# Optimization experiments

Hardware: AMD Instinct MI355X
Metric: run time of the kernel (lower is better)

## Reference

```python
import jax, jax.numpy as jnp
import numpy as np

N_F = 256
D = 4 * N_F          # d_model after PixelUnshuffle(2)
D_INNER = 2 * D      # mamba expand=2
D_STATE = 16
DT_RANK = D // 16
N_LAYERS = 8
BATCH = 16
IMG = 32


def _pixel_unshuffle(x, r):
    b, c, h, w = x.shape
    x = x.reshape(b, c, h // r, r, w // r, r)
    return x.transpose(0, 1, 3, 5, 2, 4).reshape(b, c * r * r, h // r, w // r)


def _pixel_shuffle(x, r):
    b, c, h, w = x.shape
    co = c // (r * r)
    x = x.reshape(b, co, r, r, h, w)
    return x.transpose(0, 1, 4, 2, 5, 3).reshape(b, co, h * r, w * r)


def _layernorm(x, w, b):
    mu = jnp.mean(x, -1, keepdims=True)
    var = jnp.mean((x - mu) ** 2, -1, keepdims=True)
    return (x - mu) * jax.lax.rsqrt(var + 1e-5) * w + b


def _transpose_xy(a):
    b, l, c = a.shape
    s = int(np.sqrt(l))
    return a.reshape(b, s, s, c).transpose(0, 2, 1, 3).reshape(b, l, c)


def _mamba_mixer(u, W_in_i, conv_w_i, conv_b_i, W_x_i, W_dt_i, b_dt_i, A_log_i, D_skip_i, W_out_i):
    b, l, d = u.shape
    xz = jnp.einsum('bld,ed->ble', u, W_in_i)          # (B,L,2*d_inner)
    x, z = jnp.split(xz, 2, axis=-1)
    # causal depthwise conv over sequence, kernel 4, left-pad 3
    xt = jax.lax.conv_general_dilated(
        x.transpose(0, 2, 1), conv_w_i[:, None, :], (1,), [(3, 0)],
        feature_group_count=D_INNER, dimension_numbers=('NCH', 'OIH', 'NCH'))
    x = jax.nn.silu((xt + conv_b_i[None, :, None]).transpose(0, 2, 1))  # (B,L,d_inner)
    dbc = jnp.einsum('ble,fe->blf', x, W_x_i)          # (B,L,dt_rank+2*d_state)
    dt = jax.nn.softplus(jnp.einsum('blr,er->ble', dbc[..., :DT_RANK], W_dt_i) + b_dt_i)
    Bm = dbc[..., DT_RANK:DT_RANK + D_STATE]
    Cm = dbc[..., DT_RANK + D_STATE:]
    A = -jnp.exp(A_log_i)                              # (d_inner, d_state)

    def step(h, inp):
        dt_t, B_t, C_t, x_t = inp                      # (B,di),(B,ds),(B,ds),(B,di)
        h = jnp.exp(dt_t[..., None] * A) * h + (dt_t * x_t)[..., None] * B_t[:, None, :]
        return h, jnp.einsum('bds,bs->bd', h, C_t)

    h0 = jnp.zeros((b, D_INNER, D_STATE), dtype=u.dtype)
    _, ys = jax.lax.scan(step, h0, (dt.transpose(1, 0, 2), Bm.transpose(1, 0, 2),
                                    Cm.transpose(1, 0, 2), x.transpose(1, 0, 2)))
    y = ys.transpose(1, 0, 2) + x * D_skip_i
    y = y * jax.nn.silu(z)
    return jnp.einsum('ble,de->bld', y, W_out_i)


def setup_inputs() -> dict:
    key = jax.random.key(0)
    ks = jax.random.split(key, 20)
    s = 0.02
    inp = {
        'x': jax.random.normal(ks[0], (BATCH, 3, IMG, IMG), jnp.float32),
        'noise_level': jax.random.uniform(ks[1], (BATCH, 1, 1, 1), jnp.float32),
        'pe_w1': jax.random.normal(ks[2], (N_F, 4), jnp.float32) * s,
        'pe_b1': jnp.zeros((N_F,), jnp.float32),
        'pe_w2': jax.random.normal(ks[3], (N_F, N_F), jnp.float32) * s,
        'ln_w': jnp.ones((N_LAYERS, D), jnp.float32),
        'ln_b': jnp.zeros((N_LAYERS, D), jnp.float32),
        'W_in': jax.random.normal(ks[4], (N_LAYERS, 2 * D_INNER, D), jnp.float32) * s,
        'conv_w': jax.random.normal(ks[5], (N_LAYERS, D_INNER, 4), jnp.float32) * s,
        'conv_b': jnp.zeros((N_LAYERS, D_INNER), jnp.float32),
        'W_x': jax.random.normal(ks[6], (N_LAYERS, DT_RANK + 2 * D_STATE, D_INNER), jnp.float32) * s,
        'W_dt': jax.random.normal(ks[7], (N_LAYERS, D_INNER, DT_RANK), jnp.float32) * s,
        'b_dt': jax.random.normal(ks[8], (N_LAYERS, D_INNER), jnp.float32) * s,
        'A_log': jnp.broadcast_to(jnp.log(jnp.arange(1, D_STATE + 1, dtype=jnp.float32)),
                                  (N_LAYERS, D_INNER, D_STATE)),
        'D_skip': jnp.ones((N_LAYERS, D_INNER), jnp.float32),
        'W_out': jax.random.normal(ks[9], (N_LAYERS, D, D_INNER), jnp.float32) * s,
        'op_w1': jax.random.normal(ks[10], (4 * N_F, 12 * N_F), jnp.float32) * s,
        'op_b1': jnp.zeros((4 * N_F,), jnp.float32),
        'op_w2': jax.random.normal(ks[11], (3, N_F), jnp.float32) * s,
        'op_b2': jnp.zeros((3,), jnp.float32),
    }
    return inp


def reference(x, noise_level, pe_w1, pe_b1, pe_w2, ln_w, ln_b, W_in, conv_w, conv_b,
              W_x, W_dt, b_dt, A_log, D_skip, W_out, op_w1, op_b1, op_w2, op_b2):
    B, _, H, W = x.shape
    nl = jnp.broadcast_to(noise_level, (B, 1, H, W))
    h = jnp.concatenate([x, nl], axis=1)                       # (B,4,H,W)
    h = jax.nn.relu(jnp.einsum('bchw,oc->bohw', h, pe_w1) + pe_b1[None, :, None, None])
    h = jnp.einsum('bchw,oc->bohw', h, pe_w2)
    X = _pixel_unshuffle(h, 2)                                 # (B,4*n_f,H/2,W/2)
    Bc, C, Hh, Ww = X.shape
    y = X.reshape(Bc, C, Hh * Ww).transpose(0, 2, 1)           # (B,L,d_model)
    z = None
    for i in range(N_LAYERS):
        z = y if z is None else y + z                          # Block residual routing
        yn = _layernorm(z, ln_w[i], ln_b[i])
        y = _mamba_mixer(yn, W_in[i], conv_w[i], conv_b[i], W_x[i], W_dt[i], b_dt[i],
                         A_log[i], D_skip[i], W_out[i])
        y = _transpose_xy(y)
        z = _transpose_xy(z)
        if (i + 1) % 4 == 0:
            y = y[:, ::-1]
            z = z[:, ::-1]
    y2 = y.transpose(0, 2, 1).reshape(X.shape)
    z2 = z.transpose(0, 2, 1).reshape(X.shape)
    out = jnp.concatenate([X, y2, z2], axis=1)                 # (B,12*n_f,H/2,W/2)
    out = jax.nn.relu(jnp.einsum('bchw,oc->bohw', out, op_w1) + op_b1[None, :, None, None])
    out = _pixel_shuffle(out, 2)                               # (B,n_f,H,W)
    out = jnp.einsum('bchw,oc->bohw', out, op_w2) + op_b2[None, :, None, None]
    return out
```

## Files before the change

kernel.cpp:

```cpp
#include <hip/hip_runtime.h>

typedef unsigned short u16;
typedef __bf16 bf16x8 __attribute__((ext_vector_type(8)));
typedef float f32x4 __attribute__((ext_vector_type(4)));
typedef const __attribute__((address_space(1))) void* as1p;
typedef __attribute__((address_space(3))) void* as3p;

#define VMCNT4 asm volatile("s_waitcnt vmcnt(4)" ::: "memory")
#define LGKM0  asm volatile("s_waitcnt lgkmcnt(0)" ::: "memory")

__device__ __forceinline__ float bf2f(u16 h) { return __uint_as_float(((unsigned)h) << 16); }
__device__ __forceinline__ float ldf(const void* p, size_t i, int bf) {
    return bf ? bf2f(((const u16*)p)[i]) : ((const float*)p)[i];
}
__device__ __forceinline__ float4 ldf4(const void* p, size_t i, int bf) {
    if (bf) {
        const u16* q = (const u16*)p + i;
        ushort4 v = *(const ushort4*)q;
        return make_float4(bf2f(v.x), bf2f(v.y), bf2f(v.z), bf2f(v.w));
    }
    return *(const float4*)((const float*)p + i);
}
__device__ __forceinline__ u16 f2bf(float f) {
    unsigned u = __float_as_uint(f);
    unsigned r = (u + 0x7FFFu + ((u >> 16) & 1u)) >> 16;
    return (u16)r;
}
__device__ __forceinline__ float silu_f(float x) { return x * (1.f / (1.f + __expf(-x))); }

__device__ __forceinline__ int permL(int l, int rev) {
    if (rev) l = 255 - l;
    return ((l & 15) << 4) | (l >> 4);
}

__device__ __forceinline__ void gload_lds16(const void* g, void* l) {
    __builtin_amdgcn_global_load_lds((as1p)g, (as3p)l, 16, 0, 0);
}

__global__ void k_detect(const void* lnw, int* flag) {
    if (threadIdx.x == 0 && blockIdx.x == 0) {
        unsigned w = ((const unsigned*)lnw)[0];
        *flag = (w == 0x3F803F80u) ? 1 : 0;
    }
}

__global__ void k_cvt(const void* src, size_t soff, u16* __restrict__ dst, int n,
                      const int* __restrict__ flagp) {
    int bf = *flagp;
    int i4 = (blockIdx.x * 256 + threadIdx.x) * 4;
    if (i4 >= n) return;
    float4 v = ldf4(src, soff + i4, bf);
    *(ushort4*)(dst + i4) = make_ushort4(f2bf(v.x), f2bf(v.y), f2bf(v.z), f2bf(v.w));
}

__global__ void k_cvt_padx(const void* src, u16* __restrict__ dst,
                           const int* __restrict__ flagp) {
    int bf = *flagp;
    int i4 = (blockIdx.x * 256 + threadIdx.x) * 4;
    int row = i4 >> 11, col = i4 & 2047;
    int layer = row >> 7, lrow = row & 127;
    ushort4 o = make_ushort4(0, 0, 0, 0);
    if (lrow < 96) {
        float4 v = ldf4(src, (size_t)layer * 96 * 2048 + (size_t)lrow * 2048 + col, bf);
        o = make_ushort4(f2bf(v.x), f2bf(v.y), f2bf(v.z), f2bf(v.w));
    }
    *(ushort4*)(dst + i4) = o;
}

__global__ void k_head1(const void* x, const void* nl, const void* w1, const void* b1,
                        float* __restrict__ h1, const int* flagp) {
    int bf = *flagp;
    int idx = blockIdx.x * 256 + threadIdx.x;
    int o = idx & 255, p = (idx >> 8) & 1023, b = idx >> 18;
    float c0 = ldf(x, ((size_t)b * 3 + 0) * 1024 + p, bf);
    float c1 = ldf(x, ((size_t)b * 3 + 1) * 1024 + p, bf);
    float c2 = ldf(x, ((size_t)b * 3 + 2) * 1024 + p, bf);
    float c3 = ldf(nl, b, bf);
    float acc = ldf(w1, (size_t)o * 4 + 0, bf) * c0 + ldf(w1, (size_t)o * 4 + 1, bf) * c1 +
                ldf(w1, (size_t)o * 4 + 2, bf) * c2 + ldf(w1, (size_t)o * 4 + 3, bf) * c3 +
                ldf(b1, o, bf);
    h1[idx] = fmaxf(acc, 0.f);
}

template <int EPI>
__global__ __launch_bounds__(256) void k_gemm(
    const float* __restrict__ A, int lda,
    const void* __restrict__ W, size_t woff,
    const void* __restrict__ bias, size_t boff,
    float* __restrict__ C, int N, int K,
    const int* __restrict__ flagp, int perm) {
    int bf = *flagp;
    __shared__ float As[16][68];
    __shared__ float Ws[16][68];
    int t = threadIdx.x;
    int m0 = blockIdx.y * 64, n0 = blockIdx.x * 64;
    int lrow = t >> 2, lcol = (t & 3) << 2;
    int tx = t & 15, tyr = t >> 4;
    float acc[4][4] = {};
    for (int k0 = 0; k0 < K; k0 += 16) {
        float4 av = *(const float4*)(A + (size_t)(m0 + lrow) * lda + k0 + lcol);
        float4 wv = make_float4(0.f, 0.f, 0.f, 0.f);
        int nrow = n0 + lrow;
        if (nrow < N) wv = ldf4(W, woff + (size_t)nrow * K + k0 + lcol, bf);
        __syncthreads();
        As[lcol + 0][lrow] = av.x; As[lcol + 1][lrow] = av.y;
        As[lcol + 2][lrow] = av.z; As[lcol + 3][lrow] = av.w;
        Ws[lcol + 0][lrow] = wv.x; Ws[lcol + 1][lrow] = wv.y;
        Ws[lcol + 2][lrow] = wv.z; Ws[lcol + 3][lrow] = wv.w;
        __syncthreads();
#pragma unroll
        for (int k = 0; k < 16; ++k) {
            float4 a = *(const float4*)&As[k][tyr << 2];
            float4 bv = *(const float4*)&Ws[k][tx << 2];
            float aa[4] = {a.x, a.y, a.z, a.w};
            float bb[4] = {bv.x, bv.y, bv.z, bv.w};
#pragma unroll
            for (int i = 0; i < 4; ++i)
#pragma unroll
                for (int j = 0; j < 4; ++j) acc[i][j] += aa[i] * bb[j];
        }
    }
#pragma unroll
    for (int i = 0; i < 4; ++i) {
        int m = m0 + (tyr << 2) + i;
        int mo = m;
        if (perm >= 0) { int b = m >> 8, l = m & 255; mo = (b << 8) | permL(l, perm); }
#pragma unroll
        for (int j = 0; j < 4; ++j) {
            int n = n0 + (tx << 2) + j;
            if (n >= N) continue;
            float v = acc[i][j];
            if (EPI == 1) { v += ldf(bias, boff + n, bf); v = fmaxf(v, 0.f); }
            if (EPI == 2) { v += ldf(bias, boff + n, bf); v = (v > 20.f) ? v : log1pf(expf(v)); }
            C[(size_t)mo * N + n] = v;
        }
    }
}

template <int OUT16>
__global__ __launch_bounds__(512, 2) void k_m256(
    const u16* __restrict__ A, int lda,
    const u16* __restrict__ W, int ldw,
    void* __restrict__ Cv, int ldc, int ktPerZ) {
    __shared__ __align__(16) u16 Ab[2][2][128 * 64];
    __shared__ __align__(16) u16 Bb[2][2][128 * 64];
    int t = threadIdx.x;
    int w = t >> 6, lane = t & 63;
    int wm = w >> 2, wn = w & 3;
    int fr = lane & 15, q = lane >> 4;
    int flat = blockIdx.y * gridDim.x + blockIdx.x;
    int nwg = gridDim.x * gridDim.y, cpx = nwg >> 3;
    int tile = (flat & 7) * cpx + (flat >> 3);
    int bx = tile % gridDim.x, by = tile / gridDim.x;
    int m0 = by * 256, n0 = bx * 256;
    int kt0 = blockIdx.z * ktPerZ;
    int sr = t >> 3, sslot = t & 7;

    auto stA = [&](int d, int kt, int h, int j) {
        int lr = j * 64 + sr;
        int gr = (lr >> 6) * 128 + h * 64 + (lr & 63);
        int col = kt * 64 + ((sslot ^ (lr & 7)) << 3);
        gload_lds16(A + (size_t)(m0 + gr) * lda + col, &Ab[d][h][lr * 64 + sslot * 8]);
    };
    auto stB = [&](int d, int kt, int h, int j) {
        int lr = j * 64 + sr;
        int gr = (lr >> 5) * 64 + h * 32 + (lr & 31);
        int col = kt * 64 + ((sslot ^ (lr & 7)) << 3);
        gload_lds16(W + (size_t)(n0 + gr) * ldw + col, &Bb[d][h][lr * 64 + sslot * 8]);
    };
    auto ldA = [&](int d, int mf, int kk) {
        int lr = wm * 64 + (mf & 3) * 16 + fr;
        int sl = (kk * 4 + q) ^ (lr & 7);
        return *(const bf16x8*)&Ab[d][mf >> 2][lr * 64 + sl * 8];
    };
    auto ldB = [&](int d, int nf, int kk) {
        int lr = wn * 32 + (nf & 1) * 16 + fr;
        int sl = (kk * 4 + q) ^ (lr & 7);
        return *(const bf16x8*)&Bb[d][nf >> 1][lr * 64 + sl * 8];
    };

    f32x4 acc[8][4] = {};
    bf16x8 av[4][2], bv0[2][2], bv1[2][2];

    stA(0, kt0, 0, 0); stA(0, kt0, 0, 1); stA(0, kt0, 1, 0); stA(0, kt0, 1, 1);
    stB(0, kt0, 0, 0); stB(0, kt0, 0, 1); stB(0, kt0, 1, 0); stB(0, kt0, 1, 1);
    asm volatile("s_waitcnt vmcnt(0)" ::: "memory");
    __builtin_amdgcn_s_barrier();

    for (int kt = kt0; kt < kt0 + ktPerZ; ++kt) {
        int d = (kt - kt0) & 1, nd = d ^ 1, nk = kt + 1;
        bool more = nk < kt0 + ktPerZ;
        VMCNT4;
        __builtin_amdgcn_s_barrier();
        if (more) { stA(nd, nk, 0, 0); stA(nd, nk, 0, 1); }
#pragma unroll
        for (int m = 0; m < 4; ++m) { av[m][0] = ldA(d, m, 0); av[m][1] = ldA(d, m, 1); }
#pragma unroll
        for (int n = 0; n < 2; ++n) { bv0[n][0] = ldB(d, n, 0); bv0[n][1] = ldB(d, n, 1); }
        LGKM0; __builtin_amdgcn_sched_barrier(0);
        __builtin_amdgcn_s_setprio(1);
#pragma unroll
        for (int m = 0; m < 4; ++m)
#pragma unroll
            for (int n = 0; n < 2; ++n) {
                acc[m][n] = __builtin_amdgcn_mfma_f32_16x16x32_bf16(av[m][0], bv0[n][0], acc[m][n], 0, 0, 0);
                acc[m][n] = __builtin_amdgcn_mfma_f32_16x16x32_bf16(av[m][1], bv0[n][1], acc[m][n], 0, 0, 0);
            }
        __builtin_amdgcn_s_setprio(0);
        VMCNT4;
        __builtin_amdgcn_s_barrier();
        if (more) { stB(nd, nk, 0, 0); stB(nd, nk, 0, 1); }
#pragma unroll
        for (int n = 0; n < 2; ++n) { bv1[n][0] = ldB(d, n + 2, 0); bv1[n][1] = ldB(d, n + 2, 1); }
        LGKM0; __builtin_amdgcn_sched_barrier(0);
        __builtin_amdgcn_s_setprio(1);
#pragma unroll
        for (int m = 0; m < 4; ++m)
#pragma unroll
            for (int n = 0; n < 2; ++n) {
                acc[m][n + 2] = __builtin_amdgcn_mfma_f32_16x16x32_bf16(av[m][0], bv1[n][0], acc[m][n + 2], 0, 0, 0);
                acc[m][n + 2] = __builtin_amdgcn_mfma_f32_16x16x32_bf16(av[m][1], bv1[n][1], acc[m][n + 2], 0, 0, 0);
            }
        __builtin_amdgcn_s_setprio(0);
        VMCNT4;
        __builtin_amdgcn_s_barrier();
        if (more) { stB(nd, nk, 1, 0); stB(nd, nk, 1, 1); }
#pragma unroll
        for (int m = 0; m < 4; ++m) { av[m][0] = ldA(d, m + 4, 0); av[m][1] = ldA(d, m + 4, 1); }
        LGKM0; __builtin_amdgcn_sched_barrier(0);
        __builtin_amdgcn_s_setprio(1);
#pragma unroll
        for (int m = 0; m < 4; ++m)
#pragma unroll
            for (int n = 0; n < 2; ++n) {
                acc[m + 4][n] = __builtin_amdgcn_mfma_f32_16x16x32_bf16(av[m][0], bv0[n][0], acc[m + 4][n], 0, 0, 0);
                acc[m + 4][n] = __builtin_amdgcn_mfma_f32_16x16x32_bf16(av[m][1], bv0[n][1], acc[m + 4][n], 0, 0, 0);
            }
        __builtin_amdgcn_s_setprio(0);
        VMCNT4;
        __builtin_amdgcn_s_barrier();
        if (more) { stA(nd, nk, 1, 0); stA(nd, nk, 1, 1); }
        __builtin_amdgcn_s_setprio(1);
#pragma unroll
        for (int m = 0; m < 4; ++m)
#pragma unroll
            for (int n = 0; n < 2; ++n) {
                acc[m + 4][n + 2] = __builtin_amdgcn_mfma_f32_16x16x32_bf16(av[m][0], bv1[n][0], acc[m + 4][n + 2], 0, 0, 0);
                acc[m + 4][n + 2] = __builtin_amdgcn_mfma_f32_16x16x32_bf16(av[m][1], bv1[n][1], acc[m + 4][n + 2], 0, 0, 0);
            }
        __builtin_amdgcn_s_setprio(0);
    }
    if (OUT16) {
        u16* Ch = (u16*)Cv;
#pragma unroll
        for (int m = 0; m < 8; ++m) {
            int row = m0 + wm * 128 + m * 16 + q * 4;
#pragma unroll
            for (int rr = 0; rr < 4; ++rr)
#pragma unroll
                for (int n = 0; n < 4; ++n)
                    Ch[(size_t)(row + rr) * ldc + n0 + wn * 64 + n * 16 + fr] = f2bf(acc[m][n][rr]);
        }
    } else {
        float* Cf = (float*)Cv + (size_t)blockIdx.z * (size_t)gridDim.y * 256 * ldc;
#pragma unroll
        for (int m = 0; m < 8; ++m) {
            int row = m0 + wm * 128 + m * 16 + q * 4;
#pragma unroll
            for (int rr = 0; rr < 4; ++rr)
#pragma unroll
                for (int n = 0; n < 4; ++n)
                    Cf[(size_t)(row + rr) * ldc + n0 + wn * 64 + n * 16 + fr] = acc[m][n][rr];
        }
    }
}

template <int EPI, int OUT16, int BN>
__global__ __launch_bounds__(256) void k_mgemm(
    const u16* __restrict__ A, int lda,
    const u16* __restrict__ W, int ldw,
    const void* __restrict__ bias, size_t boff,
    void* __restrict__ Cv, int ldc, int N,
    int ktPerZ, int perm, const int* __restrict__ flagp) {
    constexpr int NF = BN / 32;
    int bf = *flagp;
    __shared__ __align__(16) u16 As[128 * 32];
    __shared__ __align__(16) u16 Bs[BN * 32];
    int t = threadIdx.x;
    int gx = gridDim.x;
    int flat = blockIdx.y * gx + blockIdx.x;
    int nwg = gx * gridDim.y;
    if ((nwg & 7) == 0) {
        int cpx = nwg >> 3;
        flat = (flat & 7) * cpx + (flat >> 3);
    }
    int bx = flat % gx, by = flat / gx;
    int m0 = by * 128, n0 = bx * BN;
    int kt0 = blockIdx.z * ktPerZ;
    float* Cf = (float*)Cv + (size_t)blockIdx.z * (size_t)gridDim.y * 128 * ldc;
    u16* Ch = (u16*)Cv;
    int w = t >> 6, lane = t & 63;
    int wm = w >> 1, wn = w & 1;
    int fr = lane & 15, kb = (lane >> 4) * 8;
    int srow = lane >> 2, scol = (lane & 3) * 8;
    f32x4 acc[4][NF] = {};
    for (int kt = kt0; kt < kt0 + ktPerZ; ++kt) {
        int kc = kt * 32;
#pragma unroll
        for (int i = 0; i < 2; ++i) {
            int r = i * 64 + w * 16 + srow;
            gload_lds16(A + (size_t)(m0 + r) * lda + kc + scol, As + i * 2048 + w * 512);
        }
#pragma unroll
        for (int i = 0; i < BN / 64; ++i) {
            int r = i * 64 + w * 16 + srow;
            gload_lds16(W + (size_t)(n0 + r) * ldw + kc + scol, Bs + i * 2048 + w * 512);
        }
        __syncthreads();
        bf16x8 af[4], bv[NF];
#pragma unroll
        for (int m = 0; m < 4; ++m)
            af[m] = *(const bf16x8*)(As + (wm * 64 + m * 16 + fr) * 32 + kb);
#pragma unroll
        for (int n = 0; n < NF; ++n)
            bv[n] = *(const bf16x8*)(Bs + (wn * NF * 16 + n * 16 + fr) * 32 + kb);
#pragma unroll
        for (int m = 0; m < 4; ++m)
#pragma unroll
            for (int n = 0; n < NF; ++n)
                acc[m][n] = __builtin_amdgcn_mfma_f32_16x16x32_bf16(af[m], bv[n], acc[m][n], 0, 0, 0);
        __syncthreads();
    }
    int r0 = (lane >> 4) * 4;
#pragma unroll
    for (int m = 0; m < 4; ++m) {
        int rowb = m0 + wm * 64 + m * 16 + r0;
#pragma unroll
        for (int rr = 0; rr < 4; ++rr) {
            int row = rowb + rr;
            int mo = row;
            if (perm >= 0) { int bb = row >> 8, l = row & 255; mo = (bb << 8) | permL(l, perm); }
#pragma unroll
            for (int n = 0; n < NF; ++n) {
                int col = n0 + wn * NF * 16 + n * 16 + fr;
                if (col >= N) continue;
                float v = acc[m][n][rr];
                if (EPI == 1) { v += ldf(bias, boff + col, bf); v = fmaxf(v, 0.f); }
                if (EPI == 2) { v += ldf(bias, boff + col, bf); v = (v > 20.f) ? v : log1pf(expf(v)); }
                if (OUT16) Ch[(size_t)mo * ldc + col] = f2bf(v);
                else       Cf[(size_t)mo * ldc + col] = v;
            }
        }
    }
}

template <int EPI>
__global__ void k_ored(const float* __restrict__ part, float* __restrict__ out,
                       const void* __restrict__ bias,
                       const int* __restrict__ flagp, int perm, int nz) {
    int bf = *flagp;
    int idx4 = (blockIdx.x * 256 + threadIdx.x) * 4;
    int m = idx4 >> 10, n = idx4 & 1023;
    float4 s = make_float4(0.f, 0.f, 0.f, 0.f);
    for (int z = 0; z < nz; ++z) {
        float4 p = *(const float4*)(part + (size_t)z * 4096 * 1024 + (size_t)m * 1024 + n);
        s.x += p.x; s.y += p.y; s.z += p.z; s.w += p.w;
    }
    if (EPI == 1) {
        s.x = fmaxf(s.x + ldf(bias, n + 0, bf), 0.f);
        s.y = fmaxf(s.y + ldf(bias, n + 1, bf), 0.f);
        s.z = fmaxf(s.z + ldf(bias, n + 2, bf), 0.f);
        s.w = fmaxf(s.w + ldf(bias, n + 3, bf), 0.f);
    }
    int mo = m;
    if (perm >= 0) { int b = m >> 8, l = m & 255; mo = (b << 8) | permL(l, perm); }
    *(float4*)(out + (size_t)mo * 1024 + n) = s;
}

__global__ void k_xred(const float* __restrict__ part, float* __restrict__ dbc,
                       u16* __restrict__ dbc16) {
    int idx = blockIdx.x * 256 + threadIdx.x;
    int m = idx / 96, n = idx - m * 96;
    float s = 0.f;
#pragma unroll
    for (int z = 0; z < 8; ++z) s += part[(size_t)z * 4096 * 128 + (size_t)m * 128 + n];
    dbc[idx] = s;
    dbc16[idx] = f2bf(s);
}

__global__ void k_rearr(const float* __restrict__ h2, float* __restrict__ X) {
    int idx = blockIdx.x * 256 + threadIdx.x;
    int d = idx & 1023, l = (idx >> 10) & 255, b = idx >> 18;
    int o = d >> 2, r1 = (d >> 1) & 1, r2 = d & 1;
    int hh = l >> 4, ww = l & 15;
    int p = ((hh << 1) | r1) * 32 + ((ww << 1) | r2);
    X[idx] = h2[((size_t)b * 1024 + p) * 256 + o];
}

__global__ __launch_bounds__(256) void k_ln(
    const float* __restrict__ yin, const float* __restrict__ zold,
    float* __restrict__ znew, u16* __restrict__ yn16,
    const void* lnw, const void* lnb, size_t lno,
    const int* __restrict__ flagp, int prevPerm, int first) {
    int bf = *flagp;
    int m = blockIdx.x, b = m >> 8, l = m & 255;
    int t = threadIdx.x;
    float4 v = *(const float4*)(yin + (size_t)m * 1024 + (t << 2));
    if (!first) {
        int l2 = permL(l, prevPerm);
        float4 zv = *(const float4*)(zold + ((size_t)((b << 8) | l2)) * 1024 + (t << 2));
        v.x += zv.x; v.y += zv.y; v.z += zv.z; v.w += zv.w;
    }
    *(float4*)(znew + (size_t)m * 1024 + (t << 2)) = v;
    float s = v.x + v.y + v.z + v.w;
    float s2 = v.x * v.x + v.y * v.y + v.z * v.z + v.w * v.w;
#pragma unroll
    for (int o = 32; o > 0; o >>= 1) { s += __shfl_down(s, o, 64); s2 += __shfl_down(s2, o, 64); }
    __shared__ float red[8];
    __shared__ float mv[2];
    int wid = t >> 6;
    if ((t & 63) == 0) { red[wid] = s; red[4 + wid] = s2; }
    __syncthreads();
    if (t == 0) {
        float a = red[0] + red[1] + red[2] + red[3];
        float c = red[4] + red[5] + red[6] + red[7];
        float mu = a * (1.f / 1024.f);
        mv[0] = mu;
        mv[1] = rsqrtf(c * (1.f / 1024.f) - mu * mu + 1e-5f);
    }
    __syncthreads();
    float mu = mv[0], rs = mv[1];
    size_t wb = lno + (t << 2);
    float o0 = (v.x - mu) * rs * ldf(lnw, wb + 0, bf) + ldf(lnb, wb + 0, bf);
    float o1 = (v.y - mu) * rs * ldf(lnw, wb + 1, bf) + ldf(lnb, wb + 1, bf);
    float o2 = (v.z - mu) * rs * ldf(lnw, wb + 2, bf) + ldf(lnb, wb + 2, bf);
    float o3 = (v.w - mu) * rs * ldf(lnw, wb + 3, bf) + ldf(lnb, wb + 3, bf);
    *(ushort4*)(yn16 + (size_t)m * 1024 + (t << 2)) =
        make_ushort4(f2bf(o0), f2bf(o1), f2bf(o2), f2bf(o3));
}

__global__ void k_conv(const u16* __restrict__ xz16, const void* cw, size_t cwo,
                       const void* cb, size_t cbo,
                       u16* __restrict__ xc16, const int* __restrict__ flagp) {
    int bf = *flagp;
    int idx = blockIdx.x * 256 + threadIdx.x;
    int c = idx & 2047, l = (idx >> 11) & 255, b = idx >> 19;
    float w0 = ldf(cw, cwo + (size_t)c * 4 + 0, bf);
    float w1 = ldf(cw, cwo + (size_t)c * 4 + 1, bf);
    float w2 = ldf(cw, cwo + (size_t)c * 4 + 2, bf);
    float w3 = ldf(cw, cwo + (size_t)c * 4 + 3, bf);
    size_t base = ((size_t)b * 256) * 4096 + c;
    float acc = ldf(cb, cbo + c, bf);
    if (l >= 3) acc += w0 * bf2f(xz16[base + (size_t)(l - 3) * 4096]);
    if (l >= 2) acc += w1 * bf2f(xz16[base + (size_t)(l - 2) * 4096]);
    if (l >= 1) acc += w2 * bf2f(xz16[base + (size_t)(l - 1) * 4096]);
    acc += w3 * bf2f(xz16[base + (size_t)l * 4096]);
    xc16[idx] = f2bf(silu_f(acc));
}

__global__ __launch_bounds__(256) void k_scan_a(
    const float* __restrict__ dbc, const float* __restrict__ dt,
    const u16* __restrict__ xc16, const void* A_log, size_t ao,
    float* __restrict__ hsum, float* __restrict__ sumdt,
    const int* __restrict__ flagp) {
    int bf = *flagp;
    __shared__ float Bs[32][16];
    int t = threadIdx.x;
    int bid = blockIdx.x;
    int dg = bid & 7, ch = (bid >> 3) & 7, b = bid >> 6;
    int d = dg * 256 + t, l0 = ch * 32;
    if (t < 128) {
        int l = t >> 2, q = (t & 3) * 4;
        *(float4*)&Bs[l][q] = *(const float4*)(dbc + (size_t)(b * 256 + l0 + l) * 96 + 64 + q);
    }
    float aneg[16];
#pragma unroll
    for (int s = 0; s < 16; ++s) aneg[s] = -__expf(ldf(A_log, ao + (size_t)d * 16 + s, bf));
    float h[16];
#pragma unroll
    for (int s = 0; s < 16; ++s) h[s] = 0.f;
    float sd = 0.f;
    __syncthreads();
    const float* dtp = dt + (size_t)(b * 256 + l0) * 2048 + d;
    const u16* xp = xc16 + (size_t)(b * 256 + l0) * 2048 + d;
#pragma unroll
    for (int half = 0; half < 2; ++half) {
        float dtv[16], xv[16];
#pragma unroll
        for (int j = 0; j < 16; ++j) {
            dtv[j] = dtp[(size_t)(half * 16 + j) * 2048];
            xv[j] = bf2f(xp[(size_t)(half * 16 + j) * 2048]);
        }
#pragma unroll
        for (int j = 0; j < 16; ++j) {
            int l = half * 16 + j;
            float dx = dtv[j] * xv[j];
#pragma unroll
            for (int s = 0; s < 16; ++s) {
                float e = __expf(dtv[j] * aneg[s]);
                h[s] = e * h[s] + dx * Bs[l][s];
            }
            sd += dtv[j];
        }
    }
    size_t base = ((size_t)(b * 8 + ch) * 16) * 2048 + d;
#pragma unroll
    for (int s = 0; s < 16; ++s) hsum[base + (size_t)s * 2048] = h[s];
    sumdt[(size_t)(b * 8 + ch) * 2048 + d] = sd;
}

__global__ __launch_bounds__(256) void k_scan_c(
    const float* __restrict__ dbc, const float* __restrict__ dt,
    const u16* __restrict__ xc16, const u16* __restrict__ xz16,
    const float* __restrict__ hsum, const float* __restrict__ sumdt,
    const void* A_log, size_t ao,
    const void* Dsk, size_t doo, u16* __restrict__ ys16,
    const int* __restrict__ flagp) {
    int bf = *flagp;
    __shared__ float Bs[32][16];
    __shared__ float Cs[32][16];
    int t = threadIdx.x;
    int bid = blockIdx.x;
    int dg = bid & 7, ch = (bid >> 3) & 7, b = bid >> 6;
    int d = dg * 256 + t, l0 = ch * 32;
    if (t < 128) {
        int l = t >> 2, q = (t & 3) * 4;
        const float* row = dbc + (size_t)(b * 256 + l0 + l) * 96;
        *(float4*)&Bs[l][q] = *(const float4*)(row + 64 + q);
        *(float4*)&Cs[l][q] = *(const float4*)(row + 80 + q);
    }
    float aneg[16];
#pragma unroll
    for (int s = 0; s < 16; ++s) aneg[s] = -__expf(ldf(A_log, ao + (size_t)d * 16 + s, bf));
    float h[16];
#pragma unroll
    for (int s = 0; s < 16; ++s) h[s] = 0.f;
    for (int c = 0; c < ch; ++c) {
        float sd = sumdt[(size_t)(b * 8 + c) * 2048 + d];
        size_t hb = ((size_t)(b * 8 + c) * 16) * 2048 + d;
#pragma unroll
        for (int s = 0; s < 16; ++s)
            h[s] = __expf(aneg[s] * sd) * h[s] + hsum[hb + (size_t)s * 2048];
    }
    float Dv = ldf(Dsk, doo + d, bf);
    __syncthreads();
    const float* dtp = dt + (size_t)(b * 256 + l0) * 2048 + d;
    const u16* xp = xc16 + (size_t)(b * 256 + l0) * 2048 + d;
    const u16* zp = xz16 + (size_t)(b * 256 + l0) * 4096 + 2048 + d;
    u16* yp = ys16 + (size_t)(b * 256 + l0) * 2048 + d;
#pragma unroll
    for (int half = 0; half < 2; ++half) {
        float dtv[16], xv[16], zv[16];
#pragma unroll
        for (int j = 0; j < 16; ++j) {
            dtv[j] = dtp[(size_t)(half * 16 + j) * 2048];
            xv[j] = bf2f(xp[(size_t)(half * 16 + j) * 2048]);
            zv[j] = bf2f(zp[(size_t)(half * 16 + j) * 4096]);
        }
#pragma unroll
        for (int j = 0; j < 16; ++j) {
            int l = half * 16 + j;
            float dx = dtv[j] * xv[j];
            float acc = 0.f;
#pragma unroll
            for (int s = 0; s < 16; ++s) {
                float e = __expf(dtv[j] * aneg[s]);
                h[s] = e * h[s] + dx * Bs[l][s];
                acc += h[s] * Cs[l][s];
            }
            float v = (acc + xv[j] * Dv) * silu_f(zv[j]);
            yp[(size_t)l * 2048] = f2bf(v);
        }
    }
}

__global__ void k_concat(const float* __restrict__ X, const float* __restrict__ y,
                         const float* __restrict__ z, u16* __restrict__ cat16) {
    int idx = blockIdx.x * 256 + threadIdx.x;
    int c = idx % 3072;
    int m = idx / 3072;
    float v;
    if (c < 1024) v = X[(size_t)m * 1024 + c];
    else if (c < 2048) v = y[(size_t)m * 1024 + (c - 1024)];
    else {
        int b = m >> 8, l = m & 255;
        int l2 = permL(l, 1);
        v = z[((size_t)((b << 8) | l2)) * 1024 + (c - 2048)];
    }
    cat16[idx] = f2bf(v);
}

__global__ void k_final(const float* __restrict__ out1, const void* w2, const void* b2,
                        void* out, const int* __restrict__ flagp) {
    int bf = *flagp;
    int idx = blockIdx.x * 256 + threadIdx.x;
    int j = idx & 31, i = (idx >> 5) & 31, b = idx >> 10;
    int hh = i >> 1, r1 = i & 1, ww = j >> 1, r2 = j & 1;
    int l = (hh << 4) | ww, roff = (r1 << 1) | r2;
    const float* p = out1 + ((size_t)b * 256 + l) * 1024 + roff;
    float a0 = ldf(b2, 0, bf), a1 = ldf(b2, 1, bf), a2 = ldf(b2, 2, bf);
    for (int co = 0; co < 256; ++co) {
        float v = p[co << 2];
        a0 += v * ldf(w2, co, bf);
        a1 += v * ldf(w2, 256 + co, bf);
        a2 += v * ldf(w2, 512 + co, bf);
    }
    size_t o0 = ((size_t)b * 3) * 1024 + (i << 5) + j;
    if (bf) {
        u16* ob = (u16*)out;
        ob[o0] = f2bf(a0); ob[o0 + 1024] = f2bf(a1); ob[o0 + 2048] = f2bf(a2);
    } else {
        float* of = (float*)out;
        of[o0] = a0; of[o0 + 1024] = a1; of[o0 + 2048] = a2;
    }
}

extern "C" void kernel_launch(void* const* d_in, const int* in_sizes, int n_in,
                              void* d_out, int out_size, void* d_ws, size_t ws_size,
                              hipStream_t stream) {
    const void* I_x   = d_in[0];  const void* I_nl  = d_in[1];
    const void* I_pw1 = d_in[2];  const void* I_pb1 = d_in[3];
    const void* I_pw2 = d_in[4];  const void* I_lnw = d_in[5];
    const void* I_lnb = d_in[6];  const void* I_Win = d_in[7];
    const void* I_cw  = d_in[8];  const void* I_cb  = d_in[9];
    const void* I_Wx  = d_in[10]; const void* I_Wdt = d_in[11];
    const void* I_bdt = d_in[12]; const void* I_Alog = d_in[13];
    const void* I_Dsk = d_in[14]; const void* I_Wout = d_in[15];
    const void* I_ow1 = d_in[16]; const void* I_ob1 = d_in[17];
    const void* I_ow2 = d_in[18]; const void* I_ob2 = d_in[19];

    float* ws = (float*)d_ws;
    int* flag = (int*)d_ws;
    size_t off = 64;
    auto alloc = [&](size_t n) { float* p = ws + off; off += n; return p; };
    const size_t MD = 4096ull * 1024;
    float* Xs    = alloc(MD);
    float* y     = alloc(MD);
    float* za    = alloc(MD);
    float* zb    = alloc(MD);
    float* dbc   = alloc(4096ull * 96);
    float* dtb   = alloc(4096ull * 2048);
    float* hsum  = alloc(16ull * 8 * 16 * 2048);
    float* sumdt = alloc(16ull * 8 * 2048);
    float* opart = alloc(4ull * 4096 * 1024);
    u16* xz16  = (u16*)alloc(4096ull * 4096 / 2);
    u16* yn16  = (u16*)alloc(MD / 2);
    u16* ys16  = (u16*)alloc(MD);
    u16* xc16  = (u16*)alloc(MD);
    u16* dbc16 = (u16*)alloc(4096ull * 96 / 2);
    u16* wWin  = (u16*)alloc(8ull * 4096 * 1024 / 2);
    u16* wWx   = (u16*)alloc(8ull * 128 * 2048 / 2);
    u16* wWdt  = (u16*)alloc(8ull * 2048 * 64 / 2);
    u16* wWout = (u16*)alloc(8ull * 1024 * 2048 / 2);
    u16* wWop  = (u16*)alloc(1024ull * 3072 / 2);
    float* xpart = dtb + 4194304;
    float* h1 = dtb;
    float* out1 = y;
    u16* cat16 = yn16;
    float* h2 = y;
    float* zbufs[2] = {za, zb};

    k_detect<<<1, 64, 0, stream>>>(I_lnw, flag);

    k_cvt<<<32768, 256, 0, stream>>>(I_Win, 0, wWin, 8 * 4096 * 1024, flag);
    k_cvt_padx<<<2048, 256, 0, stream>>>(I_Wx, wWx, flag);
    k_cvt<<<1024, 256, 0, stream>>>(I_Wdt, 0, wWdt, 8 * 2048 * 64, flag);
    k_cvt<<<16384, 256, 0, stream>>>(I_Wout, 0, wWout, 8 * 1024 * 2048, flag);
    k_cvt<<<3072, 256, 0, stream>>>(I_ow1, 0, wWop, 1024 * 3072, flag);

    k_head1<<<16384, 256, 0, stream>>>(I_x, I_nl, I_pw1, I_pb1, h1, flag);
    k_gemm<0><<<dim3(4, 256), 256, 0, stream>>>(h1, 256, I_pw2, 0, nullptr, 0, h2, 256, 256, flag, -1);
    k_rearr<<<16384, 256, 0, stream>>>(h2, Xs);

    for (int i = 0; i < 8; ++i) {
        int rev = (i == 3 || i == 7) ? 1 : 0;
        int prevPerm = (i >= 1) ? ((i - 1 == 3) ? 1 : 0) : 0;
        const float* yin = (i == 0) ? Xs : y;
        float* znew = zbufs[i & 1];
        float* zold = zbufs[(i & 1) ^ 1];
        size_t ao = (size_t)i * 2048 * 16;
        k_ln<<<4096, 256, 0, stream>>>(yin, zold, znew, yn16, I_lnw, I_lnb,
                                       (size_t)i * 1024, flag, prevPerm, i == 0);
        k_m256<1><<<dim3(16, 16), 512, 0, stream>>>(
            yn16, 1024, wWin + (size_t)i * 4096 * 1024, 1024, xz16, 4096, 16);
        k_conv<<<32768, 256, 0, stream>>>(xz16, I_cw, (size_t)i * 2048 * 4, I_cb,
                                          (size_t)i * 2048, xc16, flag);
        k_mgemm<0, 0, 128><<<dim3(1, 32, 8), 256, 0, stream>>>(
            xc16, 2048, wWx + (size_t)i * 128 * 2048, 2048, nullptr, 0,
            xpart, 128, 128, 8, -1, flag);
        k_xred<<<1536, 256, 0, stream>>>(xpart, dbc, dbc16);
        k_mgemm<2, 0, 128><<<dim3(16, 32), 256, 0, stream>>>(
            dbc16, 96, wWdt + (size_t)i * 2048 * 64, 64, I_bdt, (size_t)i * 2048,
            dtb, 2048, 2048, 2, -1, flag);
        k_scan_a<<<1024, 256, 0, stream>>>(dbc, dtb, xc16, I_Alog, ao, hsum, sumdt, flag);
        k_scan_c<<<1024, 256, 0, stream>>>(dbc, dtb, xc16, xz16, hsum, sumdt, I_Alog, ao,
                                           I_Dsk, (size_t)i * 2048, ys16, flag);
        k_m256<0><<<dim3(4, 16, 4), 512, 0, stream>>>(
            ys16, 2048, wWout + (size_t)i * 1024 * 2048, 2048, opart, 1024, 8);
        k_ored<0><<<4096, 256, 0, stream>>>(opart, y, nullptr, flag, rev, 4);
    }

    k_concat<<<49152, 256, 0, stream>>>(Xs, y, zbufs[1], cat16);
    k_m256<0><<<dim3(4, 16, 4), 512, 0, stream>>>(
        cat16, 3072, wWop, 3072, opart, 1024, 12);
    k_ored<1><<<4096, 256, 0, stream>>>(opart, out1, I_ob1, flag, -1, 4);
    k_final<<<64, 256, 0, stream>>>(out1, I_ow2, I_ob2, d_out, flag);
}
```

Baseline: 2.588 ms.

## Fuse causal conv into in-proj GEMM epilogue and split-K reduce into layernorm

The in-projection GEMM now stages its bf16 output tile through shared memory and applies the causal depthwise conv plus SiLU in its epilogue for the x half, writing the z half to a separate compact buffer. This removes the standalone conv kernel and the round trip of the full xz tensor. The split-K partial sums of the out-projection are now reduced inside the next layer's layernorm kernel (with the permutation applied on read), so the separate reduce kernel runs only after the last layer. Wait counts on the final K iteration are tightened, LDS becomes one flat array that is reused for the epilogue, and the serial 128-step conv loop per thread may lengthen the GEMM tail.

```diff
diff --git a/kernel.cpp b/kernel.cpp
--- a/kernel.cpp
+++ b/kernel.cpp
@@ -7,6 +7,8 @@
 typedef __attribute__((address_space(3))) void* as3p;
 
 #define VMCNT4 asm volatile("s_waitcnt vmcnt(4)" ::: "memory")
+#define VMCNT2 asm volatile("s_waitcnt vmcnt(2)" ::: "memory")
+#define VMCNT0 asm volatile("s_waitcnt vmcnt(0)" ::: "memory")
 #define LGKM0  asm volatile("s_waitcnt lgkmcnt(0)" ::: "memory")
 
 __device__ __forceinline__ float bf2f(u16 h) { return __uint_as_float(((unsigned)h) << 16); }
@@ -137,21 +139,23 @@
     }
 }
 
-template <int OUT16>
+template <int MODE>
 __global__ __launch_bounds__(512, 2) void k_m256(
     const u16* __restrict__ A, int lda,
     const u16* __restrict__ W, int ldw,
-    void* __restrict__ Cv, int ldc, int ktPerZ) {
-    __shared__ __align__(16) u16 Ab[2][2][128 * 64];
-    __shared__ __align__(16) u16 Bb[2][2][128 * 64];
+    void* __restrict__ Cv, int ldc, int ktPerZ,
+    const void* cw, size_t cwo, const void* cb, size_t cbo,
+    u16* __restrict__ xc16, u16* __restrict__ z16,
+    const int* __restrict__ flagp) {
+    __shared__ __align__(16) u16 lds[65536];
     int t = threadIdx.x;
     int w = t >> 6, lane = t & 63;
     int wm = w >> 2, wn = w & 3;
     int fr = lane & 15, q = lane >> 4;
     int flat = blockIdx.y * gridDim.x + blockIdx.x;
     int nwg = gridDim.x * gridDim.y, cpx = nwg >> 3;
-    int tile = (flat & 7) * cpx + (flat >> 3);
-    int bx = tile % gridDim.x, by = tile / gridDim.x;
+    int tid = (flat & 7) * cpx + (flat >> 3);
+    int bx = tid % gridDim.x, by = tid / gridDim.x;
     int m0 = by * 256, n0 = bx * 256;
     int kt0 = blockIdx.z * ktPerZ;
     int sr = t >> 3, sslot = t & 7;
@@ -160,23 +164,25 @@
         int lr = j * 64 + sr;
         int gr = (lr >> 6) * 128 + h * 64 + (lr & 63);
         int col = kt * 64 + ((sslot ^ (lr & 7)) << 3);
-        gload_lds16(A + (size_t)(m0 + gr) * lda + col, &Ab[d][h][lr * 64 + sslot * 8]);
+        gload_lds16(A + (size_t)(m0 + gr) * lda + col,
+                    &lds[(d * 2 + h) * 8192 + lr * 64 + sslot * 8]);
     };
     auto stB = [&](int d, int kt, int h, int j) {
         int lr = j * 64 + sr;
         int gr = (lr >> 5) * 64 + h * 32 + (lr & 31);
         int col = kt * 64 + ((sslot ^ (lr & 7)) << 3);
-        gload_lds16(W + (size_t)(n0 + gr) * ldw + col, &Bb[d][h][lr * 64 + sslot * 8]);
+        gload_lds16(W + (size_t)(n0 + gr) * ldw + col,
+                    &lds[32768 + (d * 2 + h) * 8192 + lr * 64 + sslot * 8]);
     };
     auto ldA = [&](int d, int mf, int kk) {
         int lr = wm * 64 + (mf & 3) * 16 + fr;
         int sl = (kk * 4 + q) ^ (lr & 7);
-        return *(const bf16x8*)&Ab[d][mf >> 2][lr * 64 + sl * 8];
+        return *(const bf16x8*)&lds[(d * 2 + (mf >> 2)) * 8192 + lr * 64 + sl * 8];
     };
     auto ldB = [&](int d, int nf, int kk) {
         int lr = wn * 32 + (nf & 1) * 16 + fr;
         int sl = (kk * 4 + q) ^ (lr & 7);
-        return *(const bf16x8*)&Bb[d][nf >> 1][lr * 64 + sl * 8];
+        return *(const bf16x8*)&lds[32768 + (d * 2 + (nf >> 1)) * 8192 + lr * 64 + sl * 8];
     };
 
     f32x4 acc[8][4] = {};
@@ -184,7 +190,7 @@
 
     stA(0, kt0, 0, 0); stA(0, kt0, 0, 1); stA(0, kt0, 1, 0); stA(0, kt0, 1, 1);
     stB(0, kt0, 0, 0); stB(0, kt0, 0, 1); stB(0, kt0, 1, 0); stB(0, kt0, 1, 1);
-    asm volatile("s_waitcnt vmcnt(0)" ::: "memory");
+    VMCNT0;
     __builtin_amdgcn_s_barrier();
 
     for (int kt = kt0; kt < kt0 + ktPerZ; ++kt) {
@@ -207,7 +213,7 @@
                 acc[m][n] = __builtin_amdgcn_mfma_f32_16x16x32_bf16(av[m][1], bv0[n][1], acc[m][n], 0, 0, 0);
             }
         __builtin_amdgcn_s_setprio(0);
-        VMCNT4;
+        if (more) { VMCNT4; } else { VMCNT2; }
         __builtin_amdgcn_s_barrier();
         if (more) { stB(nd, nk, 0, 0); stB(nd, nk, 0, 1); }
 #pragma unroll
@@ -222,7 +228,7 @@
                 acc[m][n + 2] = __builtin_amdgcn_mfma_f32_16x16x32_bf16(av[m][1], bv1[n][1], acc[m][n + 2], 0, 0, 0);
             }
         __builtin_amdgcn_s_setprio(0);
-        VMCNT4;
+        if (more) { VMCNT4; } else { VMCNT0; }
         __builtin_amdgcn_s_barrier();
         if (more) { stB(nd, nk, 1, 0); stB(nd, nk, 1, 1); }
 #pragma unroll
@@ -250,8 +256,9 @@
             }
         __builtin_amdgcn_s_setprio(0);
     }
-    if (OUT16) {
-        u16* Ch = (u16*)Cv;
+
+    if (MODE == 0) {
+        float* Cf = (float*)Cv + (size_t)blockIdx.z * (size_t)gridDim.y * 256 * ldc;
 #pragma unroll
         for (int m = 0; m < 8; ++m) {
             int row = m0 + wm * 128 + m * 16 + q * 4;
@@ -259,18 +266,59 @@
             for (int rr = 0; rr < 4; ++rr)
 #pragma unroll
                 for (int n = 0; n < 4; ++n)
-                    Ch[(size_t)(row + rr) * ldc + n0 + wn * 64 + n * 16 + fr] = f2bf(acc[m][n][rr]);
+                    Cf[(size_t)(row + rr) * ldc + n0 + wn * 64 + n * 16 + fr] = acc[m][n][rr];
         }
     } else {
-        float* Cf = (float*)Cv + (size_t)blockIdx.z * (size_t)gridDim.y * 256 * ldc;
-#pragma unroll
-        for (int m = 0; m < 8; ++m) {
-            int row = m0 + wm * 128 + m * 16 + q * 4;
-#pragma unroll
-            for (int rr = 0; rr < 4; ++rr)
-#pragma unroll
-                for (int n = 0; n < 4; ++n)
-                    Cf[(size_t)(row + rr) * ldc + n0 + wn * 64 + n * 16 + fr] = acc[m][n][rr];
+        int bf = *flagp;
+        if (n0 < 2048) {
+            __syncthreads();
+#pragma unroll
+            for (int m = 0; m < 8; ++m) {
+                int row = wm * 128 + m * 16 + q * 4;
+#pragma unroll
+                for (int rr = 0; rr < 4; ++rr) {
+                    int r = row + rr, xo = ((r >> 2) & 3) << 4;
+#pragma unroll
+                    for (int n = 0; n < 4; ++n) {
+                        int c = wn * 64 + n * 16 + fr;
+                        lds[r * 256 + (c ^ xo)] = f2bf(acc[m][n][rr]);
+                    }
+                }
+            }
+            __syncthreads();
+            int col = t & 255, half = t >> 8;
+            int c = n0 + col;
+            float w0 = ldf(cw, cwo + (size_t)c * 4 + 0, bf);
+            float w1 = ldf(cw, cwo + (size_t)c * 4 + 1, bf);
+            float w2 = ldf(cw, cwo + (size_t)c * 4 + 2, bf);
+            float w3 = ldf(cw, cwo + (size_t)c * 4 + 3, bf);
+            float cbv = ldf(cb, cbo + c, bf);
+            int l0 = half * 128;
+            float x1 = 0.f, x2 = 0.f, x3 = 0.f;
+            if (l0) {
+                x1 = bf2f(lds[(l0 - 1) * 256 + (col ^ ((((l0 - 1) >> 2) & 3) << 4))]);
+                x2 = bf2f(lds[(l0 - 2) * 256 + (col ^ ((((l0 - 2) >> 2) & 3) << 4))]);
+                x3 = bf2f(lds[(l0 - 3) * 256 + (col ^ ((((l0 - 3) >> 2) & 3) << 4))]);
+            }
+            for (int r = 0; r < 128; ++r) {
+                int l = l0 + r;
+                float xv = bf2f(lds[l * 256 + (col ^ (((l >> 2) & 3) << 4))]);
+                float a = cbv + w3 * xv + w2 * x1 + w1 * x2 + w0 * x3;
+                xc16[(size_t)(m0 + l) * 2048 + c] = f2bf(silu_f(a));
+                x3 = x2; x2 = x1; x1 = xv;
+            }
+        } else {
+            int cb0 = n0 - 2048;
+#pragma unroll
+            for (int m = 0; m < 8; ++m) {
+                int row = m0 + wm * 128 + m * 16 + q * 4;
+#pragma unroll
+                for (int rr = 0; rr < 4; ++rr)
+#pragma unroll
+                    for (int n = 0; n < 4; ++n)
+                        z16[(size_t)(row + rr) * 2048 + cb0 + wn * 64 + n * 16 + fr] =
+                            f2bf(acc[m][n][rr]);
+            }
         }
     }
 }
@@ -397,19 +445,30 @@
     X[idx] = h2[((size_t)b * 1024 + p) * 256 + o];
 }
 
-__global__ __launch_bounds__(256) void k_ln(
-    const float* __restrict__ yin, const float* __restrict__ zold,
+__global__ __launch_bounds__(256) void k_lnr(
+    const float* __restrict__ yin,
+    const float* __restrict__ opart,
+    const float* __restrict__ zold,
     float* __restrict__ znew, u16* __restrict__ yn16,
     const void* lnw, const void* lnb, size_t lno,
     const int* __restrict__ flagp, int prevPerm, int first) {
     int bf = *flagp;
     int m = blockIdx.x, b = m >> 8, l = m & 255;
     int t = threadIdx.x;
-    float4 v = *(const float4*)(yin + (size_t)m * 1024 + (t << 2));
-    if (!first) {
-        int l2 = permL(l, prevPerm);
-        float4 zv = *(const float4*)(zold + ((size_t)((b << 8) | l2)) * 1024 + (t << 2));
-        v.x += zv.x; v.y += zv.y; v.z += zv.z; v.w += zv.w;
+    float4 v;
+    if (first) {
+        v = *(const float4*)(yin + (size_t)m * 1024 + (t << 2));
+    } else {
+        size_t row2 = (size_t)((b << 8) | permL(l, prevPerm)) * 1024 + (t << 2);
+        float4 p0 = *(const float4*)(opart + row2);
+        float4 p1 = *(const float4*)(opart + 4194304ull + row2);
+        float4 p2 = *(const float4*)(opart + 2ull * 4194304 + row2);
+        float4 p3 = *(const float4*)(opart + 3ull * 4194304 + row2);
+        float4 zv = *(const float4*)(zold + row2);
+        v.x = ((p0.x + p1.x) + p2.x) + p3.x + zv.x;
+        v.y = ((p0.y + p1.y) + p2.y) + p3.y + zv.y;
+        v.z = ((p0.z + p1.z) + p2.z) + p3.z + zv.z;
+        v.w = ((p0.w + p1.w) + p2.w) + p3.w + zv.w;
     }
     *(float4*)(znew + (size_t)m * 1024 + (t << 2)) = v;
     float s = v.x + v.y + v.z + v.w;
@@ -439,25 +498,6 @@
         make_ushort4(f2bf(o0), f2bf(o1), f2bf(o2), f2bf(o3));
 }
 
-__global__ void k_conv(const u16* __restrict__ xz16, const void* cw, size_t cwo,
-                       const void* cb, size_t cbo,
-                       u16* __restrict__ xc16, const int* __restrict__ flagp) {
-    int bf = *flagp;
-    int idx = blockIdx.x * 256 + threadIdx.x;
-    int c = idx & 2047, l = (idx >> 11) & 255, b = idx >> 19;
-    float w0 = ldf(cw, cwo + (size_t)c * 4 + 0, bf);
-    float w1 = ldf(cw, cwo + (size_t)c * 4 + 1, bf);
-    float w2 = ldf(cw, cwo + (size_t)c * 4 + 2, bf);
-    float w3 = ldf(cw, cwo + (size_t)c * 4 + 3, bf);
-    size_t base = ((size_t)b * 256) * 4096 + c;
-    float acc = ldf(cb, cbo + c, bf);
-    if (l >= 3) acc += w0 * bf2f(xz16[base + (size_t)(l - 3) * 4096]);
-    if (l >= 2) acc += w1 * bf2f(xz16[base + (size_t)(l - 2) * 4096]);
-    if (l >= 1) acc += w2 * bf2f(xz16[base + (size_t)(l - 1) * 4096]);
-    acc += w3 * bf2f(xz16[base + (size_t)l * 4096]);
-    xc16[idx] = f2bf(silu_f(acc));
-}
-
 __global__ __launch_bounds__(256) void k_scan_a(
     const float* __restrict__ dbc, const float* __restrict__ dt,
     const u16* __restrict__ xc16, const void* A_log, size_t ao,
@@ -511,7 +551,7 @@
 
 __global__ __launch_bounds__(256) void k_scan_c(
     const float* __restrict__ dbc, const float* __restrict__ dt,
-    const u16* __restrict__ xc16, const u16* __restrict__ xz16,
+    const u16* __restrict__ xc16, const u16* __restrict__ z16,
     const float* __restrict__ hsum, const float* __restrict__ sumdt,
     const void* A_log, size_t ao,
     const void* Dsk, size_t doo, u16* __restrict__ ys16,
@@ -546,7 +586,7 @@
     __syncthreads();
     const float* dtp = dt + (size_t)(b * 256 + l0) * 2048 + d;
     const u16* xp = xc16 + (size_t)(b * 256 + l0) * 2048 + d;
-    const u16* zp = xz16 + (size_t)(b * 256 + l0) * 4096 + 2048 + d;
+    const u16* zp = z16 + (size_t)(b * 256 + l0) * 2048 + d;
     u16* yp = ys16 + (size_t)(b * 256 + l0) * 2048 + d;
 #pragma unroll
     for (int half = 0; half < 2; ++half) {
@@ -555,7 +595,7 @@
         for (int j = 0; j < 16; ++j) {
             dtv[j] = dtp[(size_t)(half * 16 + j) * 2048];
             xv[j] = bf2f(xp[(size_t)(half * 16 + j) * 2048]);
-            zv[j] = bf2f(zp[(size_t)(half * 16 + j) * 4096]);
+            zv[j] = bf2f(zp[(size_t)(half * 16 + j) * 2048]);
         }
 #pragma unroll
         for (int j = 0; j < 16; ++j) {
@@ -643,7 +683,7 @@
     float* hsum  = alloc(16ull * 8 * 16 * 2048);
     float* sumdt = alloc(16ull * 8 * 2048);
     float* opart = alloc(4ull * 4096 * 1024);
-    u16* xz16  = (u16*)alloc(4096ull * 4096 / 2);
+    u16* z16   = (u16*)alloc(MD);
     u16* yn16  = (u16*)alloc(MD / 2);
     u16* ys16  = (u16*)alloc(MD);
     u16* xc16  = (u16*)alloc(MD);
@@ -675,16 +715,14 @@
     for (int i = 0; i < 8; ++i) {
         int rev = (i == 3 || i == 7) ? 1 : 0;
         int prevPerm = (i >= 1) ? ((i - 1 == 3) ? 1 : 0) : 0;
-        const float* yin = (i == 0) ? Xs : y;
         float* znew = zbufs[i & 1];
         float* zold = zbufs[(i & 1) ^ 1];
         size_t ao = (size_t)i * 2048 * 16;
-        k_ln<<<4096, 256, 0, stream>>>(yin, zold, znew, yn16, I_lnw, I_lnb,
-                                       (size_t)i * 1024, flag, prevPerm, i == 0);
-        k_m256<1><<<dim3(16, 16), 512, 0, stream>>>(
-            yn16, 1024, wWin + (size_t)i * 4096 * 1024, 1024, xz16, 4096, 16);
-        k_conv<<<32768, 256, 0, stream>>>(xz16, I_cw, (size_t)i * 2048 * 4, I_cb,
-                                          (size_t)i * 2048, xc16, flag);
+        k_lnr<<<4096, 256, 0, stream>>>((i == 0) ? Xs : nullptr, opart, zold, znew, yn16,
+                                        I_lnw, I_lnb, (size_t)i * 1024, flag, prevPerm, i == 0);
+        k_m256<2><<<dim3(16, 16), 512, 0, stream>>>(
+            yn16, 1024, wWin + (size_t)i * 4096 * 1024, 1024, nullptr, 0, 16,
+            I_cw, (size_t)i * 2048 * 4, I_cb, (size_t)i * 2048, xc16, z16, flag);
         k_mgemm<0, 0, 128><<<dim3(1, 32, 8), 256, 0, stream>>>(
             xc16, 2048, wWx + (size_t)i * 128 * 2048, 2048, nullptr, 0,
             xpart, 128, 128, 8, -1, flag);
@@ -693,16 +731,19 @@
             dbc16, 96, wWdt + (size_t)i * 2048 * 64, 64, I_bdt, (size_t)i * 2048,
             dtb, 2048, 2048, 2, -1, flag);
         k_scan_a<<<1024, 256, 0, stream>>>(dbc, dtb, xc16, I_Alog, ao, hsum, sumdt, flag);
-        k_scan_c<<<1024, 256, 0, stream>>>(dbc, dtb, xc16, xz16, hsum, sumdt, I_Alog, ao,
+        k_scan_c<<<1024, 256, 0, stream>>>(dbc, dtb, xc16, z16, hsum, sumdt, I_Alog, ao,
                                            I_Dsk, (size_t)i * 2048, ys16, flag);
         k_m256<0><<<dim3(4, 16, 4), 512, 0, stream>>>(
-            ys16, 2048, wWout + (size_t)i * 1024 * 2048, 2048, opart, 1024, 8);
-        k_ored<0><<<4096, 256, 0, stream>>>(opart, y, nullptr, flag, rev, 4);
+            ys16, 2048, wWout + (size_t)i * 1024 * 2048, 2048, opart, 1024, 8,
+            nullptr, 0, nullptr, 0, nullptr, nullptr, flag);
+        if (i == 7)
+            k_ored<0><<<4096, 256, 0, stream>>>(opart, y, nullptr, flag, 1, 4);
     }
 
     k_concat<<<49152, 256, 0, stream>>>(Xs, y, zbufs[1], cat16);
     k_m256<0><<<dim3(4, 16, 4), 512, 0, stream>>>(
-        cat16, 3072, wWop, 3072, opart, 1024, 12);
+        cat16, 3072, wWop, 3072, opart, 1024, 12,
+        nullptr, 0, nullptr, 0, nullptr, nullptr, flag);
     k_ored<1><<<4096, 256, 0, stream>>>(opart, out1, I_ob1, flag, -1, 4);
     k_final<<<64, 256, 0, stream>>>(out1, I_ow2, I_ob2, d_out, flag);
 }
```

Measured after the change: 2.167 ms. 1.19x faster.
